# Performance work log

Hardware: AMD Instinct MI355X
Metric: run time of the kernel (lower is better)

Reference implementation:

```python
import jax, jax.numpy as jnp
import numpy as np

D_MODEL = 1024
N_HEADS = 16
HEAD_DIM = D_MODEL // N_HEADS


def setup_inputs() -> dict:
    key = jax.random.key(0)
    ks = jax.random.split(key, 9)
    B, S = 2, 2048
    s = 1.0 / np.sqrt(D_MODEL)
    x = jax.random.normal(ks[0], (B, S, D_MODEL), dtype=jnp.float32)
    Wq = jax.random.normal(ks[1], (N_HEADS, D_MODEL, HEAD_DIM), dtype=jnp.float32) * s
    Wk = jax.random.normal(ks[2], (N_HEADS, D_MODEL, HEAD_DIM), dtype=jnp.float32) * s
    Wv = jax.random.normal(ks[3], (N_HEADS, D_MODEL, HEAD_DIM), dtype=jnp.float32) * s
    bq = jax.random.normal(ks[4], (N_HEADS, HEAD_DIM), dtype=jnp.float32) * s
    bk = jax.random.normal(ks[5], (N_HEADS, HEAD_DIM), dtype=jnp.float32) * s
    bv = jax.random.normal(ks[6], (N_HEADS, HEAD_DIM), dtype=jnp.float32) * s
    Wp = jax.random.normal(ks[7], (D_MODEL, D_MODEL), dtype=jnp.float32) * s
    bp = jax.random.normal(ks[8], (D_MODEL,), dtype=jnp.float32) * s
    return {"x": x, "Wq": Wq, "Wk": Wk, "Wv": Wv, "bq": bq, "bk": bk, "bv": bv, "Wp": Wp, "bp": bp}


def reference(x, Wq, Wk, Wv, bq, bk, bv, Wp, bp):
    # Per-head projections batched over heads: [B,S,D] x [H,D,E] -> [B,H,S,E]
    Q = jnp.einsum('bsd,hde->bhse', x, Wq) + bq[None, :, None, :]
    K = jnp.einsum('bsd,hde->bhse', x, Wk) + bk[None, :, None, :]
    V = jnp.einsum('bsd,hde->bhse', x, Wv) + bv[None, :, None, :]
    scores = jnp.einsum('bhse,bhte->bhst', Q, K) / jnp.sqrt(jnp.asarray(HEAD_DIM, x.dtype))
    attn = jax.nn.softmax(scores, axis=-1)          # [B,H,S,S]
    out = jnp.einsum('bhst,bhte->bhse', attn, V)    # [B,H,S,E]
    B, H, S, E = out.shape
    concat = out.transpose(0, 2, 1, 3).reshape(B, S, H * E)  # concat heads along feature
    return concat @ Wp.T + bp
```

## Files before the change

### kernel.cpp

```cpp
#include <hip/hip_runtime.h>
#include <hip/hip_bf16.h>

typedef __attribute__((ext_vector_type(8))) short short8;
typedef __attribute__((ext_vector_type(4))) short svec4;
typedef __attribute__((ext_vector_type(4))) float float4_t;
typedef __attribute__((ext_vector_type(8))) _Float16 half8;

#define D_MODEL 1024
#define N_HEADS 16
#define HEAD_DIM 64
#define B_SZ 2
#define SEQ 2048
#define M_ROWS (B_SZ*SEQ)
#define NQKV 3072
#define SC_LOG2E 0.18033688011112042f

__device__ __forceinline__ unsigned short f2bf(float f) {
  unsigned u = __float_as_uint(f);
  u += 0x7FFFu + ((u >> 16) & 1u);
  return (unsigned short)(u >> 16);
}

__device__ __forceinline__ unsigned short f2h(float f) {
  _Float16 h = (_Float16)f;
  return *(unsigned short*)&h;
}

__device__ __forceinline__ void gl_lds16(const unsigned short* g, unsigned short* l) {
  __builtin_amdgcn_global_load_lds(
      (const __attribute__((address_space(1))) unsigned int*)(size_t)g,
      (__attribute__((address_space(3))) unsigned int*)(unsigned int)(size_t)l,
      16, 0, 0);
}

__global__ void prep(const float* __restrict__ x, const float* __restrict__ Wp,
                     const float* __restrict__ Wq, const float* __restrict__ Wk,
                     const float* __restrict__ Wv,
                     unsigned short* __restrict__ xb, unsigned short* __restrict__ Wpb,
                     unsigned short* __restrict__ Wall) {
  __shared__ float t[16][17];
  int bid = blockIdx.x;
  if (bid < 5120) {
    const float* src; unsigned short* dst; int base;
    if (bid < 4096) { src = x;  dst = xb;  base = bid * 1024 + threadIdx.x * 4; }
    else            { src = Wp; dst = Wpb; base = (bid - 4096) * 1024 + threadIdx.x * 4; }
    float4 v = *(const float4*)(src + base);
    dst[base + 0] = f2bf(v.x);
    dst[base + 1] = f2bf(v.y);
    dst[base + 2] = f2bf(v.z);
    dst[base + 3] = f2bf(v.w);
  } else {
    int u = bid - 5120;
    int sel = u >> 12;
    u &= 4095;
    const float* W = sel == 0 ? Wq : (sel == 1 ? Wk : Wv);
    int d0 = (u & 63) * 16, e0 = ((u >> 6) & 3) * 16, hh = u >> 8;
    int tx = threadIdx.x & 15, ty = threadIdx.x >> 4;
    t[ty][tx] = W[hh * (D_MODEL * HEAD_DIM) + (d0 + ty) * HEAD_DIM + e0 + tx];
    __syncthreads();
    Wall[(size_t)(sel * 1024 + hh * 64 + e0 + ty) * D_MODEL + d0 + tx] = f2bf(t[tx][ty]);
  }
}

__global__ __launch_bounds__(256) void qkv_gemm(const unsigned short* __restrict__ xb,
                                                const unsigned short* __restrict__ Wall,
                                                const float* __restrict__ bq,
                                                const float* __restrict__ bk,
                                                const float* __restrict__ bv,
                                                unsigned short* __restrict__ Qb,
                                                unsigned short* __restrict__ Kb,
                                                unsigned short* __restrict__ Vtb) {
  __shared__ unsigned short As[128 * 32], Bs[128 * 32];
  __shared__ __align__(16) unsigned short Stage[4][16 * 72];
  const int m0 = blockIdx.x * 128, n0 = blockIdx.y * 128;
  const int lane = threadIdx.x & 63, w = threadIdx.x >> 6;
  const int l16 = lane & 15, quad = lane >> 4;
  const int wm = w & 1, wn = w >> 1;
  const int ldrow = lane >> 2, ldcol = (lane & 3) * 8;
  const unsigned short* ga0 = xb + (size_t)(m0 + w * 32 + ldrow) * D_MODEL + ldcol;
  const unsigned short* ga1 = ga0 + 16 * D_MODEL;
  const unsigned short* gb0 = Wall + (size_t)(n0 + w * 32 + ldrow) * D_MODEL + ldcol;
  const unsigned short* gb1 = gb0 + 16 * D_MODEL;
  unsigned short* lA0 = As + (w * 2 + 0) * 512;
  unsigned short* lA1 = As + (w * 2 + 1) * 512;
  unsigned short* lB0 = Bs + (w * 2 + 0) * 512;
  unsigned short* lB1 = Bs + (w * 2 + 1) * 512;
  float4_t acc[4][4];
  float4_t z = {0.f, 0.f, 0.f, 0.f};
#pragma unroll
  for (int i = 0; i < 4; i++)
#pragma unroll
    for (int j = 0; j < 4; j++) acc[i][j] = z;
  for (int k0 = 0; k0 < D_MODEL; k0 += 32) {
    __syncthreads();
    gl_lds16(ga0 + k0, lA0);
    gl_lds16(ga1 + k0, lA1);
    gl_lds16(gb0 + k0, lB0);
    gl_lds16(gb1 + k0, lB1);
    __syncthreads();
    short8 af[4], bf[4];
#pragma unroll
    for (int i = 0; i < 4; i++) af[i] = *(const short8*)&As[(wm * 64 + i * 16 + l16) * 32 + quad * 8];
#pragma unroll
    for (int j = 0; j < 4; j++) bf[j] = *(const short8*)&Bs[(wn * 64 + j * 16 + l16) * 32 + quad * 8];
#pragma unroll
    for (int i = 0; i < 4; i++)
#pragma unroll
      for (int j = 0; j < 4; j++)
        acc[i][j] = __builtin_amdgcn_mfma_f32_16x16x32_bf16(af[i], bf[j], acc[i][j], 0, 0, 0);
  }
  const int nb = n0 + wn * 64;
  const int sel = nb >> 10;
  const int h = (nb >> 6) & 15;
  const float* bias = sel == 0 ? bq : (sel == 1 ? bk : bv);
  const int mbase = m0 + wm * 64;
  const int bb = mbase >> 11;
  const size_t bh = (size_t)(bb * N_HEADS + h);
  if (sel == 2) {
    unsigned short* vs = &Stage[w][0];
    const size_t vbase = bh * (32 * 4096) + (size_t)((mbase >> 6) & 31) * 4096;
    const int e8 = lane >> 3, ch = lane & 7;
#pragma unroll
    for (int j = 0; j < 4; j++) {
      float be = bias[h * 64 + j * 16 + l16];
#pragma unroll
      for (int i = 0; i < 4; i++)
#pragma unroll
        for (int r = 0; r < 4; r++)
          vs[l16 * 72 + i * 16 + quad * 4 + r] = f2h(acc[i][j][r] + be);
#pragma unroll
      for (int rd = 0; rd < 2; rd++) {
        int er = rd * 8 + e8;
        short8 val = *(const short8*)(vs + er * 72 + ch * 8);
        *(short8*)(Vtb + vbase + (size_t)(j * 16 + er) * 64 + ch * 8) = val;
      }
    }
  } else {
    unsigned short* st = &Stage[w][0];
    unsigned short* dst = (sel == 0) ? Qb : Kb;
    const float qsc = (sel == 0) ? SC_LOG2E : 1.0f;
    const size_t rowbase = bh * SEQ + (mbase & (SEQ - 1));
    const int r2 = lane >> 1, c2 = lane & 1;
#pragma unroll
    for (int j = 0; j < 4; j++) {
      float be = bias[h * 64 + j * 16 + l16];
#pragma unroll
      for (int i = 0; i < 4; i++)
#pragma unroll
        for (int r = 0; r < 4; r++)
          st[(i * 16 + quad * 4 + r) * 18 + l16] = f2bf((acc[i][j][r] + be) * qsc);
#pragma unroll
      for (int p = 0; p < 2; p++) {
        int row = p * 32 + r2;
        short8 val = *(const short8*)(st + row * 18 + c2 * 8);
        *(short8*)(dst + (rowbase + row) * HEAD_DIM + j * 16 + c2 * 8) = val;
      }
    }
  }
}

__global__ __launch_bounds__(256) void attn_kernel(const unsigned short* __restrict__ Q,
                                                   const unsigned short* __restrict__ K,
                                                   const unsigned short* __restrict__ Vt,
                                                   unsigned short* __restrict__ concat) {
  __shared__ __align__(16) unsigned short Ks0[64 * 72], Ks1[64 * 72];
  __shared__ __align__(16) unsigned short Vs0[64 * 72], Vs1[64 * 72];
  const int b = blockIdx.z, h = blockIdx.y;
  const int tid = threadIdx.x;
  const int lane = tid & 63, w = tid >> 6;
  const int l16 = lane & 15, quad = lane >> 4;
  const size_t bh = (size_t)(b * N_HEADS + h);
  const int q0 = blockIdx.x * 128 + w * 32;
  float4_t z = {0.f, 0.f, 0.f, 0.f};

  short8 aq[2][2];
#pragma unroll
  for (int rg = 0; rg < 2; rg++)
#pragma unroll
    for (int hf = 0; hf < 2; hf++)
      aq[rg][hf] = *(const short8*)(Q + (bh * SEQ + q0 + rg * 16 + l16) * HEAD_DIM + hf * 32 + quad * 8);

  const int krow = tid >> 2, kch = (tid & 3) * 8;
  const unsigned short* kg = K + (bh * SEQ + krow) * HEAD_DIM + kch;
  const int ktw = krow * 72 + kch;
  const int vt0 = (tid & 3) * 16, vt1 = vt0 + 8;
  const unsigned short* vg = Vt + bh * (32 * 4096) + krow * 64 + vt0;
  const int tp0 = ((vt0 >> 5) << 5) + (((vt0 >> 2) & 3) << 3) + (((vt0 >> 4) & 1) << 2);
  const int tp1 = ((vt1 >> 5) << 5) + (((vt1 >> 2) & 3) << 3) + (((vt1 >> 4) & 1) << 2);
  const int vtw0 = krow * 72 + tp0, vtw1 = krow * 72 + tp1;

  float4_t o[2][4];
#pragma unroll
  for (int rg = 0; rg < 2; rg++)
#pragma unroll
    for (int ne = 0; ne < 4; ne++) o[rg][ne] = z;
  float lsp[2] = {0.f, 0.f};

  short8 kreg0 = *(const short8*)kg;
  short8 kreg1 = *(const short8*)(kg + 32);
  short8 vreg0 = *(const short8*)vg;
  short8 vreg1 = *(const short8*)(vg + 8);
  kg += 4096; vg += 4096;

  auto step = [&](unsigned short* kb, unsigned short* vb, int itv) {
    *(short8*)(kb + ktw) = kreg0;
    *(short8*)(kb + ktw + 32) = kreg1;
    svec4 a0 = {vreg0[0], vreg0[1], vreg0[2], vreg0[3]};
    svec4 a1 = {vreg0[4], vreg0[5], vreg0[6], vreg0[7]};
    svec4 b0 = {vreg1[0], vreg1[1], vreg1[2], vreg1[3]};
    svec4 b1 = {vreg1[4], vreg1[5], vreg1[6], vreg1[7]};
    *(svec4*)(vb + vtw0) = a0;
    *(svec4*)(vb + vtw0 + 8) = a1;
    *(svec4*)(vb + vtw1) = b0;
    *(svec4*)(vb + vtw1 + 8) = b1;
    __syncthreads();
    if (itv < 31) {
      kreg0 = *(const short8*)kg;
      kreg1 = *(const short8*)(kg + 32);
      vreg0 = *(const short8*)vg;
      vreg1 = *(const short8*)(vg + 8);
      kg += 4096; vg += 4096;
    }
#pragma unroll
    for (int p = 0; p < 2; p++) {
      float4_t s[2][2];
#pragma unroll
      for (int tcl = 0; tcl < 2; tcl++) {
        int tc = 2 * p + tcl;
        short8 kf0 = *(const short8*)(kb + (tc * 16 + l16) * 72 + quad * 8);
        short8 kf1 = *(const short8*)(kb + (tc * 16 + l16) * 72 + 32 + quad * 8);
#pragma unroll
        for (int rg = 0; rg < 2; rg++) {
          s[tcl][rg] = __builtin_amdgcn_mfma_f32_16x16x32_bf16(kf0, aq[rg][0], z, 0, 0, 0);
          s[tcl][rg] = __builtin_amdgcn_mfma_f32_16x16x32_bf16(kf1, aq[rg][1], s[tcl][rg], 0, 0, 0);
        }
      }
      half8 vf[4];
#pragma unroll
      for (int ne = 0; ne < 4; ne++)
        vf[ne] = *(const half8*)(vb + (ne * 16 + l16) * 72 + p * 32 + quad * 8);
#pragma unroll
      for (int rg = 0; rg < 2; rg++) {
        float pv[8];
#pragma unroll
        for (int r = 0; r < 4; r++) {
          pv[r]     = __builtin_amdgcn_exp2f(s[0][rg][r]);
          pv[4 + r] = __builtin_amdgcn_exp2f(s[1][rg][r]);
        }
        lsp[rg] += ((pv[0] + pv[1]) + (pv[2] + pv[3])) + ((pv[4] + pv[5]) + (pv[6] + pv[7]));
        half8 pa = {(_Float16)pv[0], (_Float16)pv[1], (_Float16)pv[2], (_Float16)pv[3],
                    (_Float16)pv[4], (_Float16)pv[5], (_Float16)pv[6], (_Float16)pv[7]};
#pragma unroll
        for (int ne = 0; ne < 4; ne++)
          o[rg][ne] = __builtin_amdgcn_mfma_f32_16x16x32_f16(pa, vf[ne], o[rg][ne], 0, 0, 0);
      }
    }
  };

  for (int it2 = 0; it2 < 16; ++it2) {
    step(Ks0, Vs0, 2 * it2);
    step(Ks1, Vs1, 2 * it2 + 1);
  }

  float lsf[2];
#pragma unroll
  for (int rg = 0; rg < 2; rg++) {
    float v = lsp[rg];
    v += __shfl_xor(v, 16, 64);
    v += __shfl_xor(v, 32, 64);
    lsf[rg] = v;
  }
#pragma unroll
  for (int rg = 0; rg < 2; rg++) {
#pragma unroll
    for (int r = 0; r < 4; r++) {
      float li = 1.0f / __shfl(lsf[rg], quad * 4 + r, 64);
      int sr = q0 + rg * 16 + quad * 4 + r;
#pragma unroll
      for (int ne = 0; ne < 4; ne++)
        concat[((size_t)(b * SEQ + sr)) * D_MODEL + h * 64 + ne * 16 + l16] = f2bf(o[rg][ne][r] * li);
    }
  }
}

__global__ __launch_bounds__(256) void out_gemm(const unsigned short* __restrict__ cb,
                                                const unsigned short* __restrict__ Wpb,
                                                const float* __restrict__ bp,
                                                float* __restrict__ out) {
  __shared__ unsigned short As[128 * 32], Bs[64 * 32];
  const int m0 = blockIdx.x * 128, n0 = blockIdx.y * 64;
  const int lane = threadIdx.x & 63, w = threadIdx.x >> 6;
  const int l16 = lane & 15, quad = lane >> 4;
  const int ldrow = lane >> 2, ldcol = (lane & 3) * 8;
  const unsigned short* ga0 = cb + (size_t)(m0 + w * 32 + ldrow) * D_MODEL + ldcol;
  const unsigned short* ga1 = ga0 + 16 * D_MODEL;
  const unsigned short* gb0 = Wpb + (size_t)(n0 + w * 16 + ldrow) * D_MODEL + ldcol;
  unsigned short* lA0 = As + (w * 2 + 0) * 512;
  unsigned short* lA1 = As + (w * 2 + 1) * 512;
  unsigned short* lB0 = Bs + w * 512;
  float4_t acc[2][4];
  float4_t z = {0.f, 0.f, 0.f, 0.f};
#pragma unroll
  for (int i = 0; i < 2; i++)
#pragma unroll
    for (int j = 0; j < 4; j++) acc[i][j] = z;
  for (int k0 = 0; k0 < D_MODEL; k0 += 32) {
    __syncthreads();
    gl_lds16(ga0 + k0, lA0);
    gl_lds16(ga1 + k0, lA1);
    gl_lds16(gb0 + k0, lB0);
    __syncthreads();
    short8 af[2], bf[4];
#pragma unroll
    for (int i = 0; i < 2; i++) af[i] = *(const short8*)&As[(w * 32 + i * 16 + l16) * 32 + quad * 8];
#pragma unroll
    for (int j = 0; j < 4; j++) bf[j] = *(const short8*)&Bs[(j * 16 + l16) * 32 + quad * 8];
#pragma unroll
    for (int i = 0; i < 2; i++)
#pragma unroll
      for (int j = 0; j < 4; j++)
        acc[i][j] = __builtin_amdgcn_mfma_f32_16x16x32_bf16(af[i], bf[j], acc[i][j], 0, 0, 0);
  }
#pragma unroll
  for (int i = 0; i < 2; i++)
#pragma unroll
    for (int j = 0; j < 4; j++)
#pragma unroll
      for (int r = 0; r < 4; r++) {
        int m = m0 + w * 32 + i * 16 + quad * 4 + r;
        int oc = n0 + j * 16 + l16;
        out[(size_t)m * D_MODEL + oc] = acc[i][j][r] + bp[oc];
      }
}

extern "C" void kernel_launch(void* const* d_in, const int* in_sizes, int n_in,
                              void* d_out, int out_size, void* d_ws, size_t ws_size,
                              hipStream_t stream) {
  const float* x  = (const float*)d_in[0];
  const float* Wq = (const float*)d_in[1];
  const float* Wk = (const float*)d_in[2];
  const float* Wv = (const float*)d_in[3];
  const float* bq = (const float*)d_in[4];
  const float* bk = (const float*)d_in[5];
  const float* bv = (const float*)d_in[6];
  const float* Wp = (const float*)d_in[7];
  const float* bp = (const float*)d_in[8];
  float* out = (float*)d_out;

  char* ws = (char*)d_ws;
  size_t off = 0;
  auto alloc = [&](size_t bytes) -> void* {
    void* p = ws + off;
    off += (bytes + 255) & ~(size_t)255;
    return p;
  };
  unsigned short* xb   = (unsigned short*)alloc((size_t)M_ROWS * D_MODEL * 2);
  unsigned short* Wall = (unsigned short*)alloc((size_t)NQKV * D_MODEL * 2);
  unsigned short* Wpb  = (unsigned short*)alloc((size_t)D_MODEL * D_MODEL * 2);
  unsigned short* Qb   = (unsigned short*)alloc((size_t)B_SZ * N_HEADS * SEQ * HEAD_DIM * 2);
  unsigned short* Kb   = (unsigned short*)alloc((size_t)B_SZ * N_HEADS * SEQ * HEAD_DIM * 2);
  unsigned short* Vtb  = (unsigned short*)alloc((size_t)B_SZ * N_HEADS * SEQ * HEAD_DIM * 2);
  unsigned short* cbuf = (unsigned short*)alloc((size_t)B_SZ * SEQ * D_MODEL * 2);

  prep<<<17408, 256, 0, stream>>>(x, Wp, Wq, Wk, Wv, xb, Wpb, Wall);

  qkv_gemm<<<dim3(M_ROWS / 128, NQKV / 128), 256, 0, stream>>>(xb, Wall, bq, bk, bv, Qb, Kb, Vtb);

  attn_kernel<<<dim3(SEQ / 128, N_HEADS, B_SZ), 256, 0, stream>>>(Qb, Kb, Vtb, cbuf);

  out_gemm<<<dim3(M_ROWS / 128, D_MODEL / 64), 256, 0, stream>>>(cbuf, Wpb, bp, out);
}
```

Baseline: 189.0 us.

## Split attention KV sequence across two wave groups with LDS reduction

Each attention block now runs 512 threads split into two groups. Each group processes half of the key/value sequence for the same 128 queries. The second group writes its partial outputs and row sums to shared memory, and the first group adds them and writes the normalized result. This doubles the number of waves in flight per block to hide latency, at the cost of more LDS per block, an extra reduction pass, and possibly lower block-level occupancy.

```diff
diff --git a/kernel.cpp b/kernel.cpp
--- a/kernel.cpp
+++ b/kernel.cpp
@@ -159,18 +159,22 @@
   }
 }
 
-__global__ __launch_bounds__(256) void attn_kernel(const unsigned short* __restrict__ Q,
+__global__ __launch_bounds__(512) void attn_kernel(const unsigned short* __restrict__ Q,
                                                    const unsigned short* __restrict__ K,
                                                    const unsigned short* __restrict__ Vt,
                                                    unsigned short* __restrict__ concat) {
-  __shared__ __align__(16) unsigned short Ks0[64 * 72], Ks1[64 * 72];
-  __shared__ __align__(16) unsigned short Vs0[64 * 72], Vs1[64 * 72];
+  __shared__ __align__(16) union ShU {
+    unsigned short kv[2][4][64 * 72];
+    struct { float4_t ot[4][2][4][16][4]; float ls[4][2][16]; } c;
+  } sh;
   const int b = blockIdx.z, h = blockIdx.y;
   const int tid = threadIdx.x;
   const int lane = tid & 63, w = tid >> 6;
+  const int g = w >> 2, wq = w & 3;
   const int l16 = lane & 15, quad = lane >> 4;
   const size_t bh = (size_t)(b * N_HEADS + h);
-  const int q0 = blockIdx.x * 128 + w * 32;
+  const int q0 = blockIdx.x * 128 + wq * 32;
+  const int tb = g * 1024;
   float4_t z = {0.f, 0.f, 0.f, 0.f};
 
   short8 aq[2][2];
@@ -180,11 +184,12 @@
     for (int hf = 0; hf < 2; hf++)
       aq[rg][hf] = *(const short8*)(Q + (bh * SEQ + q0 + rg * 16 + l16) * HEAD_DIM + hf * 32 + quad * 8);
 
-  const int krow = tid >> 2, kch = (tid & 3) * 8;
-  const unsigned short* kg = K + (bh * SEQ + krow) * HEAD_DIM + kch;
+  const int tl = tid & 255;
+  const int krow = tl >> 2, kch = (tl & 3) * 8;
+  const unsigned short* kg = K + (bh * SEQ + tb + krow) * HEAD_DIM + kch;
   const int ktw = krow * 72 + kch;
-  const int vt0 = (tid & 3) * 16, vt1 = vt0 + 8;
-  const unsigned short* vg = Vt + bh * (32 * 4096) + krow * 64 + vt0;
+  const int vt0 = (tl & 3) * 16, vt1 = vt0 + 8;
+  const unsigned short* vg = Vt + bh * (32 * 4096) + (size_t)(tb >> 6) * 4096 + krow * 64 + vt0;
   const int tp0 = ((vt0 >> 5) << 5) + (((vt0 >> 2) & 3) << 3) + (((vt0 >> 4) & 1) << 2);
   const int tp1 = ((vt1 >> 5) << 5) + (((vt1 >> 2) & 3) << 3) + (((vt1 >> 4) & 1) << 2);
   const int vtw0 = krow * 72 + tp0, vtw1 = krow * 72 + tp1;
@@ -214,7 +219,7 @@
     *(svec4*)(vb + vtw1) = b0;
     *(svec4*)(vb + vtw1 + 8) = b1;
     __syncthreads();
-    if (itv < 31) {
+    if (itv < 15) {
       kreg0 = *(const short8*)kg;
       kreg1 = *(const short8*)(kg + 32);
       vreg0 = *(const short8*)vg;
@@ -257,9 +262,9 @@
     }
   };
 
-  for (int it2 = 0; it2 < 16; ++it2) {
-    step(Ks0, Vs0, 2 * it2);
-    step(Ks1, Vs1, 2 * it2 + 1);
+  for (int it2 = 0; it2 < 8; ++it2) {
+    step(sh.kv[g][0], sh.kv[g][2], 2 * it2);
+    step(sh.kv[g][1], sh.kv[g][3], 2 * it2 + 1);
   }
 
   float lsf[2];
@@ -270,15 +275,34 @@
     v += __shfl_xor(v, 32, 64);
     lsf[rg] = v;
   }
-#pragma unroll
-  for (int rg = 0; rg < 2; rg++) {
-#pragma unroll
-    for (int r = 0; r < 4; r++) {
-      float li = 1.0f / __shfl(lsf[rg], quad * 4 + r, 64);
-      int sr = q0 + rg * 16 + quad * 4 + r;
-#pragma unroll
-      for (int ne = 0; ne < 4; ne++)
-        concat[((size_t)(b * SEQ + sr)) * D_MODEL + h * 64 + ne * 16 + l16] = f2bf(o[rg][ne][r] * li);
+
+  __syncthreads();
+  if (g) {
+#pragma unroll
+    for (int rg = 0; rg < 2; rg++) {
+#pragma unroll
+      for (int ne = 0; ne < 4; ne++) sh.c.ot[wq][rg][ne][l16][quad] = o[rg][ne];
+      if (quad == 0) sh.c.ls[wq][rg][l16] = lsf[rg];
+    }
+  }
+  __syncthreads();
+  if (!g) {
+#pragma unroll
+    for (int rg = 0; rg < 2; rg++) {
+      float lt = lsf[rg] + sh.c.ls[wq][rg][l16];
+#pragma unroll
+      for (int ne = 0; ne < 4; ne++) {
+        float4_t pp = sh.c.ot[wq][rg][ne][l16][quad];
+        o[rg][ne] += pp;
+      }
+#pragma unroll
+      for (int r = 0; r < 4; r++) {
+        float li = 1.0f / __shfl(lt, quad * 4 + r, 64);
+        int sr = q0 + rg * 16 + quad * 4 + r;
+#pragma unroll
+        for (int ne = 0; ne < 4; ne++)
+          concat[((size_t)(b * SEQ + sr)) * D_MODEL + h * 64 + ne * 16 + l16] = f2bf(o[rg][ne][r] * li);
+      }
     }
   }
 }
@@ -366,7 +390,7 @@
 
   qkv_gemm<<<dim3(M_ROWS / 128, NQKV / 128), 256, 0, stream>>>(xb, Wall, bq, bk, bv, Qb, Kb, Vtb);
 
-  attn_kernel<<<dim3(SEQ / 128, N_HEADS, B_SZ), 256, 0, stream>>>(Qb, Kb, Vtb, cbuf);
+  attn_kernel<<<dim3(SEQ / 128, N_HEADS, B_SZ), 512, 0, stream>>>(Qb, Kb, Vtb, cbuf);
 
   out_gemm<<<dim3(M_ROWS / 128, D_MODEL / 64), 256, 0, stream>>>(cbuf, Wpb, bp, out);
 }
```

Result: no change. 189.2 us (+0.1%).

## Split attention over key halves with a combine kernel, plus MFMA priority hints

Applied to the files above, without the earlier changes.

The attention kernel now splits each query tile's key range into two halves. Each half writes unnormalized fp32 partial outputs and row sums, and a new combine kernel adds them, normalizes and converts to bf16. The grid goes from 512 to 1024 blocks, with a remapped block index meant to spread heads across CUs and improve occupancy and load balance. It also adds s_setprio around the MFMA sections and uses packed cvt_pkrtz for the fp16 conversion. The trade-off is an extra kernel launch plus fp32 partial-output traffic, with the workspace for the partials aliased over the xb/Wall buffers, which are dead by then.

```diff
diff --git a/kernel.cpp b/kernel.cpp
--- a/kernel.cpp
+++ b/kernel.cpp
@@ -162,15 +162,20 @@
 __global__ __launch_bounds__(256) void attn_kernel(const unsigned short* __restrict__ Q,
                                                    const unsigned short* __restrict__ K,
                                                    const unsigned short* __restrict__ Vt,
-                                                   unsigned short* __restrict__ concat) {
+                                                   float* __restrict__ Op,
+                                                   float* __restrict__ Lp) {
   __shared__ __align__(16) unsigned short Ks0[64 * 72], Ks1[64 * 72];
   __shared__ __align__(16) unsigned short Vs0[64 * 72], Vs1[64 * 72];
-  const int b = blockIdx.z, h = blockIdx.y;
+  const int lin = blockIdx.x;
+  const int slot = lin >> 3;
+  const int bh = (lin & 7) * 4 + (slot >> 5);
+  const int b = bh >> 4, h = bh & 15;
+  const int th = slot & 1, qt = (slot & 31) >> 1;
   const int tid = threadIdx.x;
   const int lane = tid & 63, w = tid >> 6;
   const int l16 = lane & 15, quad = lane >> 4;
-  const size_t bh = (size_t)(b * N_HEADS + h);
-  const int q0 = blockIdx.x * 128 + w * 32;
+  const int q0 = qt * 128 + w * 32;
+  const int tb = th * 1024;
   float4_t z = {0.f, 0.f, 0.f, 0.f};
 
   short8 aq[2][2];
@@ -178,13 +183,13 @@
   for (int rg = 0; rg < 2; rg++)
 #pragma unroll
     for (int hf = 0; hf < 2; hf++)
-      aq[rg][hf] = *(const short8*)(Q + (bh * SEQ + q0 + rg * 16 + l16) * HEAD_DIM + hf * 32 + quad * 8);
+      aq[rg][hf] = *(const short8*)(Q + ((size_t)bh * SEQ + q0 + rg * 16 + l16) * HEAD_DIM + hf * 32 + quad * 8);
 
   const int krow = tid >> 2, kch = (tid & 3) * 8;
-  const unsigned short* kg = K + (bh * SEQ + krow) * HEAD_DIM + kch;
+  const unsigned short* kg = K + ((size_t)bh * SEQ + tb + krow) * HEAD_DIM + kch;
   const int ktw = krow * 72 + kch;
   const int vt0 = (tid & 3) * 16, vt1 = vt0 + 8;
-  const unsigned short* vg = Vt + bh * (32 * 4096) + krow * 64 + vt0;
+  const unsigned short* vg = Vt + (size_t)bh * (32 * 4096) + (size_t)(tb >> 6) * 4096 + krow * 64 + vt0;
   const int tp0 = ((vt0 >> 5) << 5) + (((vt0 >> 2) & 3) << 3) + (((vt0 >> 4) & 1) << 2);
   const int tp1 = ((vt1 >> 5) << 5) + (((vt1 >> 2) & 3) << 3) + (((vt1 >> 4) & 1) << 2);
   const int vtw0 = krow * 72 + tp0, vtw1 = krow * 72 + tp1;
@@ -214,7 +219,7 @@
     *(svec4*)(vb + vtw1) = b0;
     *(svec4*)(vb + vtw1 + 8) = b1;
     __syncthreads();
-    if (itv < 31) {
+    if (itv < 15) {
       kreg0 = *(const short8*)kg;
       kreg1 = *(const short8*)(kg + 32);
       vreg0 = *(const short8*)vg;
@@ -224,6 +229,7 @@
 #pragma unroll
     for (int p = 0; p < 2; p++) {
       float4_t s[2][2];
+      __builtin_amdgcn_s_setprio(1);
 #pragma unroll
       for (int tcl = 0; tcl < 2; tcl++) {
         int tc = 2 * p + tcl;
@@ -235,6 +241,7 @@
           s[tcl][rg] = __builtin_amdgcn_mfma_f32_16x16x32_bf16(kf1, aq[rg][1], s[tcl][rg], 0, 0, 0);
         }
       }
+      __builtin_amdgcn_s_setprio(0);
       half8 vf[4];
 #pragma unroll
       for (int ne = 0; ne < 4; ne++)
@@ -248,16 +255,22 @@
           pv[4 + r] = __builtin_amdgcn_exp2f(s[1][rg][r]);
         }
         lsp[rg] += ((pv[0] + pv[1]) + (pv[2] + pv[3])) + ((pv[4] + pv[5]) + (pv[6] + pv[7]));
-        half8 pa = {(_Float16)pv[0], (_Float16)pv[1], (_Float16)pv[2], (_Float16)pv[3],
-                    (_Float16)pv[4], (_Float16)pv[5], (_Float16)pv[6], (_Float16)pv[7]};
+        union { unsigned u[4]; half8 h; } pk;
+        pk.u[0] = __builtin_bit_cast(unsigned, __builtin_amdgcn_cvt_pkrtz(pv[0], pv[1]));
+        pk.u[1] = __builtin_bit_cast(unsigned, __builtin_amdgcn_cvt_pkrtz(pv[2], pv[3]));
+        pk.u[2] = __builtin_bit_cast(unsigned, __builtin_amdgcn_cvt_pkrtz(pv[4], pv[5]));
+        pk.u[3] = __builtin_bit_cast(unsigned, __builtin_amdgcn_cvt_pkrtz(pv[6], pv[7]));
+        half8 pa = pk.h;
+        __builtin_amdgcn_s_setprio(1);
 #pragma unroll
         for (int ne = 0; ne < 4; ne++)
           o[rg][ne] = __builtin_amdgcn_mfma_f32_16x16x32_f16(pa, vf[ne], o[rg][ne], 0, 0, 0);
+        __builtin_amdgcn_s_setprio(0);
       }
     }
   };
 
-  for (int it2 = 0; it2 < 16; ++it2) {
+  for (int it2 = 0; it2 < 8; ++it2) {
     step(Ks0, Vs0, 2 * it2);
     step(Ks1, Vs1, 2 * it2 + 1);
   }
@@ -270,17 +283,47 @@
     v += __shfl_xor(v, 32, 64);
     lsf[rg] = v;
   }
+
+  const size_t obase = (size_t)(th * B_SZ + b) * SEQ * D_MODEL;
 #pragma unroll
   for (int rg = 0; rg < 2; rg++) {
 #pragma unroll
     for (int r = 0; r < 4; r++) {
-      float li = 1.0f / __shfl(lsf[rg], quad * 4 + r, 64);
       int sr = q0 + rg * 16 + quad * 4 + r;
 #pragma unroll
       for (int ne = 0; ne < 4; ne++)
-        concat[((size_t)(b * SEQ + sr)) * D_MODEL + h * 64 + ne * 16 + l16] = f2bf(o[rg][ne][r] * li);
+        Op[obase + (size_t)sr * D_MODEL + h * 64 + ne * 16 + l16] = o[rg][ne][r];
     }
   }
+  if (quad == 0) {
+#pragma unroll
+    for (int rg = 0; rg < 2; rg++)
+      Lp[(size_t)(th * 32 + bh) * SEQ + q0 + rg * 16 + l16] = lsf[rg];
+  }
+}
+
+__global__ __launch_bounds__(256) void combine(const float* __restrict__ Op,
+                                               const float* __restrict__ Lp,
+                                               unsigned short* __restrict__ cb) {
+  const int r = blockIdx.x * 2 + (threadIdx.x >> 7);
+  const int c0 = (threadIdx.x & 127) * 8;
+  const int b = r >> 11, s = r & (SEQ - 1), h = c0 >> 6;
+  const float l0 = Lp[(size_t)(b * N_HEADS + h) * SEQ + s];
+  const float l1 = Lp[(size_t)(32 + b * N_HEADS + h) * SEQ + s];
+  const float sc = 1.0f / (l0 + l1);
+  const float* p0 = Op + ((size_t)b * SEQ + s) * D_MODEL + c0;
+  const float* p1 = p0 + (size_t)B_SZ * SEQ * D_MODEL;
+  float4_t a0 = *(const float4_t*)p0;
+  float4_t a1 = *(const float4_t*)(p0 + 4);
+  float4_t b0 = *(const float4_t*)p1;
+  float4_t b1 = *(const float4_t*)(p1 + 4);
+  short8 o;
+#pragma unroll
+  for (int j = 0; j < 4; j++) {
+    o[j]     = (short)f2bf((a0[j] + b0[j]) * sc);
+    o[4 + j] = (short)f2bf((a1[j] + b1[j]) * sc);
+  }
+  *(short8*)(cb + (size_t)r * D_MODEL + c0) = o;
 }
 
 __global__ __launch_bounds__(256) void out_gemm(const unsigned short* __restrict__ cb,
@@ -354,19 +397,25 @@
     off += (bytes + 255) & ~(size_t)255;
     return p;
   };
-  unsigned short* xb   = (unsigned short*)alloc((size_t)M_ROWS * D_MODEL * 2);
-  unsigned short* Wall = (unsigned short*)alloc((size_t)NQKV * D_MODEL * 2);
-  unsigned short* Wpb  = (unsigned short*)alloc((size_t)D_MODEL * D_MODEL * 2);
   unsigned short* Qb   = (unsigned short*)alloc((size_t)B_SZ * N_HEADS * SEQ * HEAD_DIM * 2);
   unsigned short* Kb   = (unsigned short*)alloc((size_t)B_SZ * N_HEADS * SEQ * HEAD_DIM * 2);
   unsigned short* Vtb  = (unsigned short*)alloc((size_t)B_SZ * N_HEADS * SEQ * HEAD_DIM * 2);
+  unsigned short* Wpb  = (unsigned short*)alloc((size_t)D_MODEL * D_MODEL * 2);
   unsigned short* cbuf = (unsigned short*)alloc((size_t)B_SZ * SEQ * D_MODEL * 2);
+  size_t offA = off;
+  unsigned short* xb   = (unsigned short*)alloc((size_t)M_ROWS * D_MODEL * 2);
+  unsigned short* Wall = (unsigned short*)alloc((size_t)NQKV * D_MODEL * 2);
+  off = offA;
+  float* Opart = (float*)alloc((size_t)2 * B_SZ * SEQ * D_MODEL * 4);
+  float* Lpart = (float*)alloc((size_t)2 * B_SZ * N_HEADS * SEQ * 4);
 
   prep<<<17408, 256, 0, stream>>>(x, Wp, Wq, Wk, Wv, xb, Wpb, Wall);
 
   qkv_gemm<<<dim3(M_ROWS / 128, NQKV / 128), 256, 0, stream>>>(xb, Wall, bq, bk, bv, Qb, Kb, Vtb);
 
-  attn_kernel<<<dim3(SEQ / 128, N_HEADS, B_SZ), 256, 0, stream>>>(Qb, Kb, Vtb, cbuf);
+  attn_kernel<<<1024, 256, 0, stream>>>(Qb, Kb, Vtb, Opart, Lpart);
+
+  combine<<<M_ROWS / 2, 256, 0, stream>>>(Opart, Lpart, cbuf);
 
   out_gemm<<<dim3(M_ROWS / 128, D_MODEL / 64), 256, 0, stream>>>(cbuf, Wpb, bp, out);
 }
```

After: 197.0 us. +4.2%, slower.

## Enlarge attention query tile, remap blocks per XCD, add setprio and packed converts

Applied to the files above, without the earlier changes.

Each wave in the attention kernel now handles 64 query rows instead of 32, so a block covers 256 queries. This halves how many times K/V tiles are loaded and staged through LDS per query. The grid becomes a 1D launch of 256 blocks, with a mapping that places all blocks of a given (batch, head) on the same XCD for L2 locality. The change also wraps the MFMA groups in s_setprio and replaces scalar fp16 conversions with cvt_pkrtz packed conversions. In exchange, register pressure rises, the block count drops to 256, which may leave some CUs idle, and round-toward-zero changes the precision of the P values.

```diff
diff --git a/kernel.cpp b/kernel.cpp
--- a/kernel.cpp
+++ b/kernel.cpp
@@ -165,36 +165,39 @@
                                                    unsigned short* __restrict__ concat) {
   __shared__ __align__(16) unsigned short Ks0[64 * 72], Ks1[64 * 72];
   __shared__ __align__(16) unsigned short Vs0[64 * 72], Vs1[64 * 72];
-  const int b = blockIdx.z, h = blockIdx.y;
+  const int lin = blockIdx.x;
+  const int xcd = lin & 7, slot = lin >> 3;
+  const int bh = xcd * 4 + (slot >> 3);
+  const int b = bh >> 4, h = bh & 15;
+  const int qt = slot & 7;
   const int tid = threadIdx.x;
   const int lane = tid & 63, w = tid >> 6;
   const int l16 = lane & 15, quad = lane >> 4;
-  const size_t bh = (size_t)(b * N_HEADS + h);
-  const int q0 = blockIdx.x * 128 + w * 32;
+  const int q0 = qt * 256 + w * 64;
   float4_t z = {0.f, 0.f, 0.f, 0.f};
 
-  short8 aq[2][2];
-#pragma unroll
-  for (int rg = 0; rg < 2; rg++)
+  short8 aq[4][2];
+#pragma unroll
+  for (int rg = 0; rg < 4; rg++)
 #pragma unroll
     for (int hf = 0; hf < 2; hf++)
-      aq[rg][hf] = *(const short8*)(Q + (bh * SEQ + q0 + rg * 16 + l16) * HEAD_DIM + hf * 32 + quad * 8);
+      aq[rg][hf] = *(const short8*)(Q + ((size_t)bh * SEQ + q0 + rg * 16 + l16) * HEAD_DIM + hf * 32 + quad * 8);
 
   const int krow = tid >> 2, kch = (tid & 3) * 8;
-  const unsigned short* kg = K + (bh * SEQ + krow) * HEAD_DIM + kch;
+  const unsigned short* kg = K + ((size_t)bh * SEQ + krow) * HEAD_DIM + kch;
   const int ktw = krow * 72 + kch;
   const int vt0 = (tid & 3) * 16, vt1 = vt0 + 8;
-  const unsigned short* vg = Vt + bh * (32 * 4096) + krow * 64 + vt0;
+  const unsigned short* vg = Vt + (size_t)bh * (32 * 4096) + krow * 64 + vt0;
   const int tp0 = ((vt0 >> 5) << 5) + (((vt0 >> 2) & 3) << 3) + (((vt0 >> 4) & 1) << 2);
   const int tp1 = ((vt1 >> 5) << 5) + (((vt1 >> 2) & 3) << 3) + (((vt1 >> 4) & 1) << 2);
   const int vtw0 = krow * 72 + tp0, vtw1 = krow * 72 + tp1;
 
-  float4_t o[2][4];
-#pragma unroll
-  for (int rg = 0; rg < 2; rg++)
+  float4_t o[4][4];
+#pragma unroll
+  for (int rg = 0; rg < 4; rg++)
 #pragma unroll
     for (int ne = 0; ne < 4; ne++) o[rg][ne] = z;
-  float lsp[2] = {0.f, 0.f};
+  float lsp[4] = {0.f, 0.f, 0.f, 0.f};
 
   short8 kreg0 = *(const short8*)kg;
   short8 kreg1 = *(const short8*)(kg + 32);
@@ -223,36 +226,44 @@
     }
 #pragma unroll
     for (int p = 0; p < 2; p++) {
-      float4_t s[2][2];
+      short8 kf[2][2];
 #pragma unroll
       for (int tcl = 0; tcl < 2; tcl++) {
         int tc = 2 * p + tcl;
-        short8 kf0 = *(const short8*)(kb + (tc * 16 + l16) * 72 + quad * 8);
-        short8 kf1 = *(const short8*)(kb + (tc * 16 + l16) * 72 + 32 + quad * 8);
-#pragma unroll
-        for (int rg = 0; rg < 2; rg++) {
-          s[tcl][rg] = __builtin_amdgcn_mfma_f32_16x16x32_bf16(kf0, aq[rg][0], z, 0, 0, 0);
-          s[tcl][rg] = __builtin_amdgcn_mfma_f32_16x16x32_bf16(kf1, aq[rg][1], s[tcl][rg], 0, 0, 0);
-        }
+        kf[tcl][0] = *(const short8*)(kb + (tc * 16 + l16) * 72 + quad * 8);
+        kf[tcl][1] = *(const short8*)(kb + (tc * 16 + l16) * 72 + 32 + quad * 8);
       }
       half8 vf[4];
 #pragma unroll
       for (int ne = 0; ne < 4; ne++)
         vf[ne] = *(const half8*)(vb + (ne * 16 + l16) * 72 + p * 32 + quad * 8);
 #pragma unroll
-      for (int rg = 0; rg < 2; rg++) {
+      for (int rg = 0; rg < 4; rg++) {
+        float4_t s0, s1;
+        __builtin_amdgcn_s_setprio(1);
+        s0 = __builtin_amdgcn_mfma_f32_16x16x32_bf16(kf[0][0], aq[rg][0], z, 0, 0, 0);
+        s0 = __builtin_amdgcn_mfma_f32_16x16x32_bf16(kf[0][1], aq[rg][1], s0, 0, 0, 0);
+        s1 = __builtin_amdgcn_mfma_f32_16x16x32_bf16(kf[1][0], aq[rg][0], z, 0, 0, 0);
+        s1 = __builtin_amdgcn_mfma_f32_16x16x32_bf16(kf[1][1], aq[rg][1], s1, 0, 0, 0);
+        __builtin_amdgcn_s_setprio(0);
         float pv[8];
 #pragma unroll
         for (int r = 0; r < 4; r++) {
-          pv[r]     = __builtin_amdgcn_exp2f(s[0][rg][r]);
-          pv[4 + r] = __builtin_amdgcn_exp2f(s[1][rg][r]);
+          pv[r]     = __builtin_amdgcn_exp2f(s0[r]);
+          pv[4 + r] = __builtin_amdgcn_exp2f(s1[r]);
         }
         lsp[rg] += ((pv[0] + pv[1]) + (pv[2] + pv[3])) + ((pv[4] + pv[5]) + (pv[6] + pv[7]));
-        half8 pa = {(_Float16)pv[0], (_Float16)pv[1], (_Float16)pv[2], (_Float16)pv[3],
-                    (_Float16)pv[4], (_Float16)pv[5], (_Float16)pv[6], (_Float16)pv[7]};
+        union { unsigned u[4]; half8 h; } pk;
+        pk.u[0] = __builtin_bit_cast(unsigned, __builtin_amdgcn_cvt_pkrtz(pv[0], pv[1]));
+        pk.u[1] = __builtin_bit_cast(unsigned, __builtin_amdgcn_cvt_pkrtz(pv[2], pv[3]));
+        pk.u[2] = __builtin_bit_cast(unsigned, __builtin_amdgcn_cvt_pkrtz(pv[4], pv[5]));
+        pk.u[3] = __builtin_bit_cast(unsigned, __builtin_amdgcn_cvt_pkrtz(pv[6], pv[7]));
+        half8 pa = pk.h;
+        __builtin_amdgcn_s_setprio(1);
 #pragma unroll
         for (int ne = 0; ne < 4; ne++)
           o[rg][ne] = __builtin_amdgcn_mfma_f32_16x16x32_f16(pa, vf[ne], o[rg][ne], 0, 0, 0);
+        __builtin_amdgcn_s_setprio(0);
       }
     }
   };
@@ -262,16 +273,16 @@
     step(Ks1, Vs1, 2 * it2 + 1);
   }
 
-  float lsf[2];
-#pragma unroll
-  for (int rg = 0; rg < 2; rg++) {
+  float lsf[4];
+#pragma unroll
+  for (int rg = 0; rg < 4; rg++) {
     float v = lsp[rg];
     v += __shfl_xor(v, 16, 64);
     v += __shfl_xor(v, 32, 64);
     lsf[rg] = v;
   }
 #pragma unroll
-  for (int rg = 0; rg < 2; rg++) {
+  for (int rg = 0; rg < 4; rg++) {
 #pragma unroll
     for (int r = 0; r < 4; r++) {
       float li = 1.0f / __shfl(lsf[rg], quad * 4 + r, 64);
@@ -366,7 +377,7 @@
 
   qkv_gemm<<<dim3(M_ROWS / 128, NQKV / 128), 256, 0, stream>>>(xb, Wall, bq, bk, bv, Qb, Kb, Vtb);
 
-  attn_kernel<<<dim3(SEQ / 128, N_HEADS, B_SZ), 256, 0, stream>>>(Qb, Kb, Vtb, cbuf);
+  attn_kernel<<<256, 256, 0, stream>>>(Qb, Kb, Vtb, cbuf);
 
   out_gemm<<<dim3(M_ROWS / 128, D_MODEL / 64), 256, 0, stream>>>(cbuf, Wpb, bp, out);
 }
```

Measured after the change: 190.4 us. About the same (+0.7%).
